# Performance work log

Measured on AMD Instinct MI355X. Metric: run time of the kernel, lower is better.

Reference implementation:

```python
import jax, jax.numpy as jnp
import numpy as np

B, K, L = 512, 256, 1000   # batch, n_kernels, embedding input length (input_size - kw + 1)
E = 3                      # per-kernel embedding dim
OUT = 128                  # output_size


def setup_inputs() -> dict:
    key = jax.random.key(0)
    k1, k2, k3, k4 = jax.random.split(key, 4)
    x = jax.random.normal(k1, (B, K, L), dtype=jnp.float32)
    # nn.Linear(L, 3, bias=False) -> weight [3, L]
    W_emb = jax.random.normal(k2, (E, L), dtype=jnp.float32) * (1.0 / np.sqrt(L))
    # nn.Linear(3*K, OUT) -> weight [OUT, 3*K], bias [OUT]
    W_fc2 = jax.random.normal(k3, (OUT, E * K), dtype=jnp.float32) * (1.0 / np.sqrt(E * K))
    b_fc2 = jax.random.normal(k4, (OUT,), dtype=jnp.float32) * 0.01
    return {"x": x, "W_emb": W_emb, "W_fc2": W_fc2, "b_fc2": b_fc2}


def reference(x, W_emb, W_fc2, b_fc2):
    # Batched form of the per-(sample, kernel) Linear: y[b,k] = W_emb @ x[b,k]
    y = jnp.einsum('bkl,el->bke', x, W_emb)          # [B, K, 3]
    y = y.reshape(x.shape[0], -1)                     # [B, 3*K] (kernel-major, matches torch .view)
    return y @ W_fc2.T + b_fc2                        # [B, OUT]
```

## Files before the change

### kernel.cpp

```cpp
#include <hip/hip_runtime.h>
#include <hip/hip_bf16.h>

#define BATCH 512
#define NKER  256
#define LEN   1000
#define EDIM  3
#define OUTN  128
#define NROWS (BATCH * NKER)
#define NF4   (LEN / 4)
#define FC_IN (EDIM * NKER)

typedef float fv4 __attribute__((ext_vector_type(4)));

#define DOT4(a, w) ((a)[0]*(w)[0] + (a)[1]*(w)[1] + (a)[2]*(w)[2] + (a)[3]*(w)[3])

__global__ __launch_bounds__(256) void stage1_emb(const float* __restrict__ x,
                                                  const float* __restrict__ W_emb,
                                                  float* __restrict__ y) {
    __shared__ float w_s[EDIM][LEN];
    for (int i = threadIdx.x; i < EDIM * LEN; i += 256) {
        w_s[i / LEN][i % LEN] = W_emb[i];
    }
    __syncthreads();

    const int wave = threadIdx.x >> 6;
    const int lane = threadIdx.x & 63;
    const int gw = blockIdx.x * 4 + wave;

    const bool tail = (lane < NF4 - 192);
    const int f3 = tail ? (lane + 192) : 0;
    const fv4 z4 = {0.f, 0.f, 0.f, 0.f};

    const fv4* w0p = reinterpret_cast<const fv4*>(&w_s[0][0]);
    const fv4* w1p = reinterpret_cast<const fv4*>(&w_s[1][0]);
    const fv4* w2p = reinterpret_cast<const fv4*>(&w_s[2][0]);

    #pragma unroll 1
    for (int i = 0; i < 8; ++i) {
        const int rowA = gw * 2 + i * 16384;
        const fv4* xa = reinterpret_cast<const fv4*>(x + (size_t)rowA * LEN);
        const fv4* xb = reinterpret_cast<const fv4*>(x + (size_t)(rowA + 1) * LEN);

        fv4 a0 = __builtin_nontemporal_load(&xa[lane]);
        fv4 a1 = __builtin_nontemporal_load(&xa[lane + 64]);
        fv4 a2 = __builtin_nontemporal_load(&xa[lane + 128]);
        fv4 a3 = tail ? __builtin_nontemporal_load(&xa[lane + 192]) : z4;
        fv4 b0 = __builtin_nontemporal_load(&xb[lane]);
        fv4 b1 = __builtin_nontemporal_load(&xb[lane + 64]);
        fv4 b2 = __builtin_nontemporal_load(&xb[lane + 128]);
        fv4 b3 = tail ? __builtin_nontemporal_load(&xb[lane + 192]) : z4;

        float sA0, sA1, sA2, sB0, sB1, sB2;
        {
            fv4 w;
            w = w0p[lane];       sA0  = DOT4(a0, w);  sB0  = DOT4(b0, w);
            w = w1p[lane];       sA1  = DOT4(a0, w);  sB1  = DOT4(b0, w);
            w = w2p[lane];       sA2  = DOT4(a0, w);  sB2  = DOT4(b0, w);
            w = w0p[lane + 64];  sA0 += DOT4(a1, w);  sB0 += DOT4(b1, w);
            w = w1p[lane + 64];  sA1 += DOT4(a1, w);  sB1 += DOT4(b1, w);
            w = w2p[lane + 64];  sA2 += DOT4(a1, w);  sB2 += DOT4(b1, w);
            w = w0p[lane + 128]; sA0 += DOT4(a2, w);  sB0 += DOT4(b2, w);
            w = w1p[lane + 128]; sA1 += DOT4(a2, w);  sB1 += DOT4(b2, w);
            w = w2p[lane + 128]; sA2 += DOT4(a2, w);  sB2 += DOT4(b2, w);
            w = w0p[f3];         sA0 += DOT4(a3, w);  sB0 += DOT4(b3, w);
            w = w1p[f3];         sA1 += DOT4(a3, w);  sB1 += DOT4(b3, w);
            w = w2p[f3];         sA2 += DOT4(a3, w);  sB2 += DOT4(b3, w);
        }

        #pragma unroll
        for (int m = 32; m >= 1; m >>= 1) {
            sA0 += __shfl_xor(sA0, m);
            sA1 += __shfl_xor(sA1, m);
            sA2 += __shfl_xor(sA2, m);
            sB0 += __shfl_xor(sB0, m);
            sB1 += __shfl_xor(sB1, m);
            sB2 += __shfl_xor(sB2, m);
        }
        if (lane == 0) {
            float* yr = y + (size_t)rowA * EDIM;
            yr[0] = sA0;
            yr[1] = sA1;
            yr[2] = sA2;
            yr[3] = sB0;
            yr[4] = sB1;
            yr[5] = sB2;
        }
    }
}

__global__ __launch_bounds__(256) void transpose_wfc2(const float* __restrict__ W,
                                                      float* __restrict__ Wt) {
    int idx = blockIdx.x * 256 + threadIdx.x;
    if (idx < FC_IN * OUTN) {
        int j = idx >> 7;
        int o = idx & (OUTN - 1);
        Wt[idx] = W[o * FC_IN + j];
    }
}

__global__ __launch_bounds__(256) void stage2_fc(const float* __restrict__ y,
                                                 const float* __restrict__ Wt,
                                                 const float* __restrict__ bias,
                                                 float* __restrict__ out) {
    __shared__ float ys[FC_IN];
    __shared__ float part[OUTN];
    const int b = blockIdx.x;
    for (int i = threadIdx.x; i < FC_IN; i += 256) ys[i] = y[(size_t)b * FC_IN + i];
    __syncthreads();

    const int o = threadIdx.x & (OUTN - 1);
    const int h = threadIdx.x >> 7;
    const int j0 = h * (FC_IN / 2);
    float acc = 0.f;
    #pragma unroll 8
    for (int j = j0; j < j0 + FC_IN / 2; ++j) {
        acc += ys[j] * Wt[j * OUTN + o];
    }
    if (h) part[o] = acc;
    __syncthreads();
    if (!h) out[(size_t)b * OUTN + o] = acc + part[o] + bias[o];
}

extern "C" void kernel_launch(void* const* d_in, const int* in_sizes, int n_in,
                              void* d_out, int out_size, void* d_ws, size_t ws_size,
                              hipStream_t stream) {
    const float* x     = (const float*)d_in[0];
    const float* W_emb = (const float*)d_in[1];
    const float* W_fc2 = (const float*)d_in[2];
    const float* b_fc2 = (const float*)d_in[3];
    float* out = (float*)d_out;

    float* y  = (float*)d_ws;
    float* Wt = y + (size_t)NROWS * EDIM;

    transpose_wfc2<<<(FC_IN * OUTN + 255) / 256, 256, 0, stream>>>(W_fc2, Wt);

    stage1_emb<<<2048, 256, 0, stream>>>(x, W_emb, y);

    stage2_fc<<<BATCH, 256, 0, stream>>>(y, Wt, b_fc2, out);
}
```

Measured before the change: 111.2 us.

## Defer cross-lane reduction of embedding dots to the FC stage

Stage 1 now reduces each row's partial dot products only across groups of 8 lanes (three shuffle rounds instead of six). Eight lanes per wave write 6 partial sums each into a partial buffer. Stage 2 loads those partials per batch sample into shared memory and finishes the 8-way sum before the FC matmul. This cuts shuffle work in the bandwidth-bound stage 1, in exchange for 8x more intermediate writes and reads plus extra shared memory in stage 2.

```diff
diff --git a/kernel.cpp b/kernel.cpp
--- a/kernel.cpp
+++ b/kernel.cpp
@@ -7,8 +7,10 @@
 #define EDIM  3
 #define OUTN  128
 #define NROWS (BATCH * NKER)
+#define NPAIRS (NROWS / 2)
 #define NF4   (LEN / 4)
 #define FC_IN (EDIM * NKER)
+#define PREC  48
 
 typedef float fv4 __attribute__((ext_vector_type(4)));
 
@@ -16,7 +18,7 @@
 
 __global__ __launch_bounds__(256) void stage1_emb(const float* __restrict__ x,
                                                   const float* __restrict__ W_emb,
-                                                  float* __restrict__ y) {
+                                                  float* __restrict__ ypart) {
     __shared__ float w_s[EDIM][LEN];
     for (int i = threadIdx.x; i < EDIM * LEN; i += 256) {
         w_s[i / LEN][i % LEN] = W_emb[i];
@@ -68,7 +70,7 @@
         }
 
         #pragma unroll
-        for (int m = 32; m >= 1; m >>= 1) {
+        for (int m = 1; m <= 4; m <<= 1) {
             sA0 += __shfl_xor(sA0, m);
             sA1 += __shfl_xor(sA1, m);
             sA2 += __shfl_xor(sA2, m);
@@ -76,14 +78,14 @@
             sB1 += __shfl_xor(sB1, m);
             sB2 += __shfl_xor(sB2, m);
         }
-        if (lane == 0) {
-            float* yr = y + (size_t)rowA * EDIM;
-            yr[0] = sA0;
-            yr[1] = sA1;
-            yr[2] = sA2;
-            yr[3] = sB0;
-            yr[4] = sB1;
-            yr[5] = sB2;
+        if ((lane & 7) == 0) {
+            float* pr = ypart + (size_t)(rowA >> 1) * PREC + (lane >> 3) * 6;
+            pr[0] = sA0;
+            pr[1] = sA1;
+            pr[2] = sA2;
+            pr[3] = sB0;
+            pr[4] = sB1;
+            pr[5] = sB2;
         }
     }
 }
@@ -98,14 +100,27 @@
     }
 }
 
-__global__ __launch_bounds__(256) void stage2_fc(const float* __restrict__ y,
+__global__ __launch_bounds__(256) void stage2_fc(const float* __restrict__ ypart,
                                                  const float* __restrict__ Wt,
                                                  const float* __restrict__ bias,
                                                  float* __restrict__ out) {
+    __shared__ float tile[128 * PREC];
     __shared__ float ys[FC_IN];
     __shared__ float part[OUTN];
     const int b = blockIdx.x;
-    for (int i = threadIdx.x; i < FC_IN; i += 256) ys[i] = y[(size_t)b * FC_IN + i];
+
+    const fv4* src = reinterpret_cast<const fv4*>(ypart + (size_t)b * 128 * PREC);
+    fv4* dst = reinterpret_cast<fv4*>(tile);
+    for (int i = threadIdx.x; i < 128 * PREC / 4; i += 256) dst[i] = src[i];
+    __syncthreads();
+
+    for (int j = threadIdx.x; j < FC_IN; j += 256) {
+        const int k = j / 3;
+        const int e = j - k * 3;
+        const float* tp = &tile[(k >> 1) * PREC + (k & 1) * 3 + e];
+        ys[j] = ((tp[0] + tp[6]) + (tp[12] + tp[18])) +
+                ((tp[24] + tp[30]) + (tp[36] + tp[42]));
+    }
     __syncthreads();
 
     const int o = threadIdx.x & (OUTN - 1);
@@ -130,12 +145,12 @@
     const float* b_fc2 = (const float*)d_in[3];
     float* out = (float*)d_out;
 
-    float* y  = (float*)d_ws;
-    float* Wt = y + (size_t)NROWS * EDIM;
+    float* ypart = (float*)d_ws;
+    float* Wt = ypart + (size_t)NPAIRS * PREC;
 
     transpose_wfc2<<<(FC_IN * OUTN + 255) / 256, 256, 0, stream>>>(W_fc2, Wt);
 
-    stage1_emb<<<2048, 256, 0, stream>>>(x, W_emb, y);
+    stage1_emb<<<2048, 256, 0, stream>>>(x, W_emb, ypart);
 
-    stage2_fc<<<BATCH, 256, 0, stream>>>(y, Wt, b_fc2, out);
+    stage2_fc<<<BATCH, 256, 0, stream>>>(ypart, Wt, b_fc2, out);
 }
```

Result: slower. 125.2 us (+12.6%).
